# Kernel optimization log

Measured on AMD Instinct MI355X. Metric: run time of the kernel, lower is better.

The kernel has to match this reference:

```python
import jax, jax.numpy as jnp
import numpy as np


def conv2d(x, w, pad=1):
    return jax.lax.conv_general_dilated(
        x, w, (1, 1), [(pad, pad), (pad, pad)],
        dimension_numbers=('NCHW', 'OIHW', 'NCHW'))


def bn(x, g, b, m, v, eps=1e-5):
    inv = g / jnp.sqrt(v + eps)
    return x * inv[None, :, None, None] + (b - m * inv)[None, :, None, None]


def deform_conv(x, wp, bp, wd):
    # v2-style DeformConv2D: internal p_conv -> offsets, bilinear sample, 3x3 conv
    b, c, h, w = x.shape
    ks = 3
    N = ks * ks
    offset = conv2d(x, wp, 1) + bp[None, :, None, None]   # (b, 2N, h, w)
    xp = jnp.pad(x, ((0, 0), (0, 0), (1, 1), (1, 1)))     # zero_padding(1)
    Hp, Wp = h + 2, w + 2
    off = offset.transpose(0, 2, 3, 1)                    # (b, h, w, 2N)
    pn_y, pn_x = jnp.meshgrid(jnp.arange(-1, 2), jnp.arange(-1, 2), indexing='ij')
    # sampling locations p = p_0 + p_n + offset (in padded coords)
    py = jnp.arange(1, h + 1)[None, :, None, None] + pn_y.reshape(-1)[None, None, None, :] + off[..., :N]
    px = jnp.arange(1, w + 1)[None, None, :, None] + pn_x.reshape(-1)[None, None, None, :] + off[..., N:]
    fy = jnp.floor(jax.lax.stop_gradient(py))
    fx = jnp.floor(jax.lax.stop_gradient(px))
    qy0 = jnp.clip(fy, 0, Hp - 1); qy1 = jnp.clip(fy + 1, 0, Hp - 1)
    qx0 = jnp.clip(fx, 0, Wp - 1); qx1 = jnp.clip(fx + 1, 0, Wp - 1)
    py = jnp.clip(py, 0, Hp - 1); px = jnp.clip(px, 0, Wp - 1)
    g_lt = (1 + (qy0 - py)) * (1 + (qx0 - px))
    g_rb = (1 - (qy1 - py)) * (1 - (qx1 - px))
    g_lb = (1 + (qy0 - py)) * (1 - (qx1 - px))
    g_rt = (1 - (qy1 - py)) * (1 + (qx0 - px))
    flat = xp.reshape(b, c, Hp * Wp)

    def gather(qy, qx):
        idx = (qy * Wp + qx).astype(jnp.int32).reshape(b, 1, -1)
        return jnp.take_along_axis(flat, idx, axis=2).reshape(b, c, h, w, N)

    x_off = (g_lt[:, None] * gather(qy0, qx0) + g_rb[:, None] * gather(qy1, qx1)
             + g_lb[:, None] * gather(qy0, qx1) + g_rt[:, None] * gather(qy1, qx0))
    outc = wd.shape[0]
    # equivalent to _reshape_x_offset + Conv2d(kernel=ks, stride=ks)
    return jnp.einsum('bchwn,ocn->bohw', x_off, wd.reshape(outc, c, N))


def setup_inputs() -> dict:
    key = jax.random.key(0)
    ks = jax.random.split(key, 24)
    B, H, W = 256, 28, 28

    def nrm(k, s, sc=1.0):
        return jax.random.normal(k, s, jnp.float32) * sc

    return {
        'x': nrm(ks[0], (B, 3, H, W)),
        'w1': nrm(ks[1], (32, 3, 3, 3), 0.2),
        'g1': jax.random.uniform(ks[2], (32,), jnp.float32) + 0.5,
        'b1': nrm(ks[3], (32,), 0.1),
        'm1': nrm(ks[4], (32,), 0.1),
        'v1': jax.random.uniform(ks[5], (32,), jnp.float32) + 0.5,
        'wp': nrm(ks[6], (18, 32, 3, 3), 0.01),  # p_conv: small offsets
        'bp': nrm(ks[7], (18,), 0.1),
        'w2': nrm(ks[8], (32, 32, 3, 3), 0.1),
        'g2': jax.random.uniform(ks[9], (32,), jnp.float32) + 0.5,
        'b2': nrm(ks[10], (32,), 0.1),
        'm2': nrm(ks[11], (32,), 0.1),
        'v2': jax.random.uniform(ks[12], (32,), jnp.float32) + 0.5,
        'w3': nrm(ks[13], (64, 32, 3, 3), 0.1),
        'g3': jax.random.uniform(ks[14], (64,), jnp.float32) + 0.5,
        'b3': nrm(ks[15], (64,), 0.1),
        'm3': nrm(ks[16], (64,), 0.1),
        'v3': jax.random.uniform(ks[17], (64,), jnp.float32) + 0.5,
        'wc': nrm(ks[18], (10, 64), 0.1),
        'bc': nrm(ks[19], (10,), 0.1),
    }


def reference(x, w1, g1, b1, m1, v1, wp, bp, w2, g2, b2, m2, v2,
              w3, g3, b3, m3, v3, wc, bc):
    h = bn(jax.nn.relu(conv2d(x, w1)), g1, b1, m1, v1)
    h = bn(jax.nn.relu(deform_conv(h, wp, bp, w2)), g2, b2, m2, v2)
    h = bn(jax.nn.relu(conv2d(h, w3)), g3, b3, m3, v3)
    h = h.mean(axis=(2, 3))               # avg_pool2d(28) on 28x28 -> global mean
    logits = h @ wc.T + bc
    return jax.nn.log_softmax(logits, axis=1)
```

## Files before the change

kernel.cpp:

```cpp
#include <hip/hip_runtime.h>
#include <hip/hip_bf16.h>
#include <math.h>

typedef __attribute__((ext_vector_type(8))) short short8;
typedef __attribute__((ext_vector_type(4))) float floatx4;
typedef __attribute__((ext_vector_type(2))) float floatx2;

#define NB 256

#define WPB_OFF 0u
#define W2B_OFF 18432u
#define W3B_OFF 36864u
#define W1B_OFF 73728u
#define C1S_OFF 75776u
#define C2S_OFF 75904u
#define C3S_OFF 76032u

#define L_IMG1 0
#define L_U    50240
#define L_OFFT 100480
#define L_WL   114304
#define L_TOT  152192

static __device__ __forceinline__ unsigned short f2bf(float f) {
    unsigned u = __float_as_uint(f);
    u = (u + 0x7fffu + ((u >> 16) & 1u)) >> 16;
    return (unsigned short)u;
}

static __device__ __forceinline__ unsigned pk2bf(float a, float b) {
    __hip_bfloat162 h = __float22bfloat162_rn(make_float2(a, b));
    unsigned r;
    __builtin_memcpy(&r, &h, 4);
    return r;
}

static __device__ __forceinline__ floatx2 up2(unsigned u) {
    floatx2 r;
    r.x = __uint_as_float(u << 16);
    r.y = __uint_as_float(u & 0xffff0000u);
    return r;
}

__global__ void wcvt(const float* __restrict__ wp, const float* __restrict__ w2,
                     const float* __restrict__ w3, const float* __restrict__ w1,
                     const float* __restrict__ g1, const float* __restrict__ b1,
                     const float* __restrict__ m1, const float* __restrict__ v1,
                     const float* __restrict__ g2, const float* __restrict__ b2,
                     const float* __restrict__ m2, const float* __restrict__ v2,
                     const float* __restrict__ g3, const float* __restrict__ b3,
                     const float* __restrict__ m3, const float* __restrict__ v3,
                     unsigned short* __restrict__ wpb, unsigned short* __restrict__ w2b,
                     unsigned short* __restrict__ w3b, unsigned short* __restrict__ w1b,
                     float* __restrict__ c1s, float* __restrict__ c2s,
                     float* __restrict__ c3s)
{
    int t = blockIdx.x * 256 + threadIdx.x;
    if (t < 9216) {
        int oc = t / 288, k = t % 288;
        int n = k >> 5, ic = k & 31;
        wpb[t] = (oc < 18) ? f2bf(wp[oc * 288 + ic * 9 + n]) : (unsigned short)0;
    } else if (t < 18432) {
        int i = t - 9216;
        int oc = i / 288, k = i % 288;
        int n = k >> 5, ic = k & 31;
        float inv = g2[oc] * rsqrtf(v2[oc] + 1e-5f);
        w2b[i] = f2bf(w2[oc * 288 + ic * 9 + n] * inv);
    } else if (t < 36864) {
        int i = t - 18432;
        int oc = i / 288, k = i % 288;
        int n = k >> 5, ic = k & 31;
        float inv = g3[oc] * rsqrtf(v3[oc] + 1e-5f);
        w3b[i] = f2bf(w3[oc * 288 + ic * 9 + n] * inv);
    } else if (t < 37888) {
        int i = t - 36864;
        int oc = i >> 5, k = i & 31;
        int n = k / 3, ic = k - n * 3;
        float inv = g1[oc] * rsqrtf(v1[oc] + 1e-5f);
        w1b[i] = (k < 27) ? f2bf(w1[oc * 27 + ic * 9 + n] * inv) : (unsigned short)0;
    } else if (t < 37920) {
        int c = t - 37888;
        float inv = g1[c] * rsqrtf(v1[c] + 1e-5f);
        c1s[c] = b1[c] - m1[c] * inv;
    } else if (t < 37952) {
        int c = t - 37920;
        float inv = g2[c] * rsqrtf(v2[c] + 1e-5f);
        c2s[c] = b2[c] - m2[c] * inv;
    } else if (t < 38016) {
        int c = t - 37952;
        float inv = g3[c] * rsqrtf(v3[c] + 1e-5f);
        c3s[c] = b3[c] - m3[c] * inv;
    }
}

__global__ __launch_bounds__(768, 3) void meganet(
    const float* __restrict__ x,
    const unsigned short* __restrict__ wpb, const unsigned short* __restrict__ w2b,
    const unsigned short* __restrict__ w3b, const unsigned short* __restrict__ w1b,
    const float* __restrict__ c1s, const float* __restrict__ c2s,
    const float* __restrict__ c3s, const float* __restrict__ bp,
    const float* __restrict__ wc, const float* __restrict__ bc,
    float* __restrict__ outp)
{
    __shared__ __align__(16) unsigned char ALL[L_TOT];
    int t = threadIdx.x, b = blockIdx.x;
    int w = t >> 6, l = t & 63, col = l & 15, q = l >> 4;

    unsigned char* img1 = ALL + L_IMG1;
    unsigned char* uimg = ALL + L_U;

    {
        const float4* xg = (const float4*)(x + (size_t)b * 2352);
        float4* xl = (float4*)uimg;
        for (int i = t; i < 588; i += 768) xl[i] = xg[i];
    }
    {
        const uint4* s1 = (const uint4*)wpb;
        const uint4* s2 = (const uint4*)w2b;
        for (int i = t; i < 2304; i += 768) {
            int row = i / 36, g = i - row * 36;
            uint4 v = (row < 32) ? s1[row * 36 + g] : s2[(row - 32) * 36 + g];
            *(uint4*)(ALL + L_WL + row * 592 + g * 16) = v;
        }
        if (t < 128) *(uint4*)(ALL + L_OFFT + t * 16) = ((const uint4*)w1b)[t];
    }
    if (t == 700) ((float*)uimg)[2352] = 0.f;
    if (t < 4)  *(uint4*)(img1 + 784 * 64 + t * 16) = make_uint4(0u, 0u, 0u, 0u);
    if (t >= 4 && t < 8) *(uint4*)(uimg + 784 * 64 + (t - 4) * 16) = make_uint4(0u, 0u, 0u, 0u);

    float s0 = c1s[col], s1v = c1s[16 + col];
    float bias0 = bp[col];
    float bias1 = (col < 2) ? bp[16 + col] : 0.f;
    float sh0 = c2s[col], sh1 = c2s[16 + col];

    __syncthreads();

    {
        short8 bf0 = *(const short8*)(ALL + L_OFFT + col * 64 + q * 16);
        short8 bf1 = *(const short8*)(ALL + L_OFFT + (16 + col) * 64 + q * 16);
        const float* xs = (const float*)uimg;
        for (int mt = w; mt < 49; mt += 12) {
            int p = mt * 16 + col;
            int y = p / 28, xx = p % 28;
            unsigned au[4];
#pragma unroll
            for (int jp = 0; jp < 4; jp++) {
                float vv[2];
#pragma unroll
                for (int h = 0; h < 2; h++) {
                    int k = q * 8 + jp * 2 + h;
                    int n = k / 3, ic = k - n * 3;
                    int yy = y + n / 3 - 1, xc = xx + n % 3 - 1;
                    bool ok = (k < 27) && ((unsigned)yy < 28u) && ((unsigned)xc < 28u);
                    int idx = ok ? (ic * 784 + yy * 28 + xc) : 2352;
                    vv[h] = xs[idx];
                }
                au[jp] = pk2bf(vv[0], vv[1]);
            }
            uint4 a4 = make_uint4(au[0], au[1], au[2], au[3]);
            short8 a = *(short8*)&a4;
            floatx4 d0 = {0.f, 0.f, 0.f, 0.f}, d1 = {0.f, 0.f, 0.f, 0.f};
            d0 = __builtin_amdgcn_mfma_f32_16x16x32_bf16(a, bf0, d0, 0, 0, 0);
            d1 = __builtin_amdgcn_mfma_f32_16x16x32_bf16(a, bf1, d1, 0, 0, 0);
#pragma unroll
            for (int r = 0; r < 4; r++) {
                int pout = mt * 16 + q * 4 + r;
                *(unsigned short*)(img1 + pout * 64 + col * 2) = f2bf(fmaxf(d0[r], 0.f) + s0);
                *(unsigned short*)(img1 + pout * 64 + 32 + col * 2) = f2bf(fmaxf(d1[r], 0.f) + s1v);
            }
        }
    }
    __syncthreads();

    {
        const unsigned char* ib = img1;
        float* otw = (float*)(ALL + L_OFFT) + w * 288;

        for (int mt = w; mt < 49; mt += 12) {
            int p = mt * 16 + col;
            int y = p / 28, xx = p % 28;

            floatx4 a0 = {0.f, 0.f, 0.f, 0.f}, a1 = {0.f, 0.f, 0.f, 0.f};
#pragma unroll
            for (int n = 0; n < 9; n++) {
                int yy = y + n / 3 - 1, xc = xx + n % 3 - 1;
                bool ok = ((unsigned)yy < 28u) && ((unsigned)xc < 28u);
                int tp = ok ? (yy * 28 + xc) : 784;
                short8 a  = *(const short8*)(ib + tp * 64 + q * 16);
                short8 p0 = *(const short8*)(ALL + L_WL + col * 592 + n * 64 + q * 16);
                short8 p1 = *(const short8*)(ALL + L_WL + (16 + col) * 592 + n * 64 + q * 16);
                a0 = __builtin_amdgcn_mfma_f32_16x16x32_bf16(a, p0, a0, 0, 0, 0);
                a1 = __builtin_amdgcn_mfma_f32_16x16x32_bf16(a, p1, a1, 0, 0, 0);
            }
#pragma unroll
            for (int r = 0; r < 4; r++)
                otw[(q * 4 + r) * 18 + col] = a0[r] + bias0;
            if (col < 2) {
#pragma unroll
                for (int r = 0; r < 4; r++)
                    otw[(q * 4 + r) * 18 + 16 + col] = a1[r] + bias1;
            }
            __asm__ volatile("s_waitcnt lgkmcnt(0)" ::: "memory");

            floatx4 d0 = {0.f, 0.f, 0.f, 0.f}, d1 = {0.f, 0.f, 0.f, 0.f};
#pragma unroll
            for (int n = 0; n < 9; n++) {
                float offy = otw[col * 18 + n];
                float offx = otw[col * 18 + 9 + n];
                float py = (float)(y + n / 3) + offy;
                float px = (float)(xx + n % 3) + offx;
                float fy = floorf(py), fx = floorf(px);
                float qy0 = fminf(fmaxf(fy, 0.f), 29.f);
                float qy1 = fminf(fmaxf(fy + 1.f, 0.f), 29.f);
                float qx0 = fminf(fmaxf(fx, 0.f), 29.f);
                float qx1 = fminf(fmaxf(fx + 1.f, 0.f), 29.f);
                float pyc = fminf(fmaxf(py, 0.f), 29.f);
                float pxc = fminf(fmaxf(px, 0.f), 29.f);
                float glt = (1.f + (qy0 - pyc)) * (1.f + (qx0 - pxc));
                float grb = (1.f - (qy1 - pyc)) * (1.f - (qx1 - pxc));
                float glb = (1.f + (qy0 - pyc)) * (1.f - (qx1 - pxc));
                float grt = (1.f - (qy1 - pyc)) * (1.f + (qx0 - pxc));
                int iy0 = (int)qy0, iy1 = (int)qy1, ix0 = (int)qx0, ix1 = (int)qx1;
                int ly0 = iy0 - 1, ly1 = iy1 - 1, lx0 = ix0 - 1, lx1 = ix1 - 1;
                bool v00 = ((unsigned)ly0 < 28u) && ((unsigned)lx0 < 28u);
                bool v11 = ((unsigned)ly1 < 28u) && ((unsigned)lx1 < 28u);
                bool v01 = ((unsigned)ly0 < 28u) && ((unsigned)lx1 < 28u);
                bool v10 = ((unsigned)ly1 < 28u) && ((unsigned)lx0 < 28u);
                int p00 = v00 ? (ly0 * 28 + lx0) : 784;
                int p11 = v11 ? (ly1 * 28 + lx1) : 784;
                int p01 = v01 ? (ly0 * 28 + lx1) : 784;
                int p10 = v10 ? (ly1 * 28 + lx0) : 784;
                uint4 u00 = *(const uint4*)(ib + p00 * 64 + q * 16);
                uint4 u11 = *(const uint4*)(ib + p11 * 64 + q * 16);
                uint4 u01 = *(const uint4*)(ib + p01 * 64 + q * 16);
                uint4 u10 = *(const uint4*)(ib + p10 * 64 + q * 16);
                floatx2 f0 = up2(u00.x) * glt + up2(u11.x) * grb + up2(u01.x) * glb + up2(u10.x) * grt;
                floatx2 f1 = up2(u00.y) * glt + up2(u11.y) * grb + up2(u01.y) * glb + up2(u10.y) * grt;
                floatx2 f2 = up2(u00.z) * glt + up2(u11.z) * grb + up2(u01.z) * glb + up2(u10.z) * grt;
                floatx2 f3 = up2(u00.w) * glt + up2(u11.w) * grb + up2(u01.w) * glb + up2(u10.w) * grt;
                uint4 af4 = make_uint4(pk2bf(f0.x, f0.y), pk2bf(f1.x, f1.y),
                                       pk2bf(f2.x, f2.y), pk2bf(f3.x, f3.y));
                short8 af = *(short8*)&af4;
                short8 wb0 = *(const short8*)(ALL + L_WL + (32 + col) * 592 + n * 64 + q * 16);
                short8 wb1 = *(const short8*)(ALL + L_WL + (48 + col) * 592 + n * 64 + q * 16);
                d0 = __builtin_amdgcn_mfma_f32_16x16x32_bf16(af, wb0, d0, 0, 0, 0);
                d1 = __builtin_amdgcn_mfma_f32_16x16x32_bf16(af, wb1, d1, 0, 0, 0);
            }
#pragma unroll
            for (int r = 0; r < 4; r++) {
                int pout = mt * 16 + q * 4 + r;
                *(unsigned short*)(uimg + pout * 64 + col * 2) = f2bf(fmaxf(d0[r], 0.f) + sh0);
                *(unsigned short*)(uimg + pout * 64 + 32 + col * 2) = f2bf(fmaxf(d1[r], 0.f) + sh1);
            }
        }
    }
    __syncthreads();

    {
        const uint4* src = (const uint4*)w3b;
        for (int i = t; i < 2304; i += 768) {
            int row = i / 36, g = i - row * 36;
            *(uint4*)(ALL + L_WL + row * 592 + g * 16) = src[row * 36 + g];
        }
    }
    __syncthreads();

    {
        float* part = (float*)(ALL + L_OFFT);
        int ocp = w & 1;
        const unsigned char* ib = uimg;
        float psA = 0.f, psB = 0.f;
        for (int mt = (w >> 1); mt < 49; mt += 6) {
            int p = mt * 16 + col;
            int y = p / 28, xx = p % 28;
            floatx4 cA = {0.f, 0.f, 0.f, 0.f}, cB = {0.f, 0.f, 0.f, 0.f};
#pragma unroll
            for (int n = 0; n < 9; n++) {
                int yy = y + n / 3 - 1, xc = xx + n % 3 - 1;
                bool ok = ((unsigned)yy < 28u) && ((unsigned)xc < 28u);
                int tp = ok ? (yy * 28 + xc) : 784;
                short8 a  = *(const short8*)(ib + tp * 64 + q * 16);
                short8 wA = *(const short8*)(ALL + L_WL + (ocp * 32 + col) * 592 + n * 64 + q * 16);
                short8 wB = *(const short8*)(ALL + L_WL + (ocp * 32 + 16 + col) * 592 + n * 64 + q * 16);
                cA = __builtin_amdgcn_mfma_f32_16x16x32_bf16(a, wA, cA, 0, 0, 0);
                cB = __builtin_amdgcn_mfma_f32_16x16x32_bf16(a, wB, cB, 0, 0, 0);
            }
            psA += fmaxf(cA[0], 0.f) + fmaxf(cA[1], 0.f) + fmaxf(cA[2], 0.f) + fmaxf(cA[3], 0.f);
            psB += fmaxf(cB[0], 0.f) + fmaxf(cB[1], 0.f) + fmaxf(cB[2], 0.f) + fmaxf(cB[3], 0.f);
        }
        psA += __shfl_xor(psA, 16, 64); psA += __shfl_xor(psA, 32, 64);
        psB += __shfl_xor(psB, 16, 64); psB += __shfl_xor(psB, 32, 64);
        if (l < 16) { part[w * 32 + l] = psA; part[w * 32 + 16 + l] = psB; }
    }
    __syncthreads();

    if (t < 64) {
        const float* part = (const float*)(ALL + L_OFFT);
        int hi = t >> 5, c = t & 31;
        float s = 0.f;
#pragma unroll
        for (int j = 0; j < 6; j++) s += part[(2 * j + hi) * 32 + c];
        float feat = s * (1.f / 784.f) + c3s[t];
        float lg[10];
        float mx = -1e30f;
#pragma unroll
        for (int j = 0; j < 10; j++) {
            float v = feat * wc[j * 64 + t];
            v += __shfl_xor(v, 1, 64);  v += __shfl_xor(v, 2, 64);
            v += __shfl_xor(v, 4, 64);  v += __shfl_xor(v, 8, 64);
            v += __shfl_xor(v, 16, 64); v += __shfl_xor(v, 32, 64);
            lg[j] = v + bc[j];
            mx = fmaxf(mx, lg[j]);
        }
        float se = 0.f;
#pragma unroll
        for (int j = 0; j < 10; j++) se += expf(lg[j] - mx);
        float lse = logf(se);
#pragma unroll
        for (int j = 0; j < 10; j++)
            if (t == j) outp[(size_t)b * 10 + j] = lg[j] - mx - lse;
    }
}

extern "C" void kernel_launch(void* const* d_in, const int* in_sizes, int n_in,
                              void* d_out, int out_size, void* d_ws, size_t ws_size,
                              hipStream_t stream)
{
    (void)in_sizes; (void)n_in; (void)out_size; (void)ws_size;
    const float* x  = (const float*)d_in[0];
    const float* w1 = (const float*)d_in[1];
    const float* g1 = (const float*)d_in[2];
    const float* b1 = (const float*)d_in[3];
    const float* m1 = (const float*)d_in[4];
    const float* v1 = (const float*)d_in[5];
    const float* wp = (const float*)d_in[6];
    const float* bp = (const float*)d_in[7];
    const float* w2 = (const float*)d_in[8];
    const float* g2 = (const float*)d_in[9];
    const float* b2 = (const float*)d_in[10];
    const float* m2 = (const float*)d_in[11];
    const float* v2 = (const float*)d_in[12];
    const float* w3 = (const float*)d_in[13];
    const float* g3 = (const float*)d_in[14];
    const float* b3 = (const float*)d_in[15];
    const float* m3 = (const float*)d_in[16];
    const float* v3 = (const float*)d_in[17];
    const float* wc = (const float*)d_in[18];
    const float* bc = (const float*)d_in[19];
    float* outp = (float*)d_out;

    unsigned char* ws = (unsigned char*)d_ws;
    unsigned short* wpb = (unsigned short*)(ws + WPB_OFF);
    unsigned short* w2b = (unsigned short*)(ws + W2B_OFF);
    unsigned short* w3b = (unsigned short*)(ws + W3B_OFF);
    unsigned short* w1b = (unsigned short*)(ws + W1B_OFF);
    float* c1s = (float*)(ws + C1S_OFF);
    float* c2s = (float*)(ws + C2S_OFF);
    float* c3s = (float*)(ws + C3S_OFF);

    wcvt<<<149, 256, 0, stream>>>(wp, w2, w3, w1, g1, b1, m1, v1,
                                  g2, b2, m2, v2, g3, b3, m3, v3,
                                  wpb, w2b, w3b, w1b, c1s, c2s, c3s);
    meganet<<<NB, 768, 0, stream>>>(x, wpb, w2b, w3b, w1b, c1s, c2s, c3s,
                                    bp, wc, bc, outp);
}
```

Measured before the change: 138.5 us.

## Deduplicate bilinear coordinate math across quad lanes via LDS records

```diff
diff --git a/kernel.cpp b/kernel.cpp
--- a/kernel.cpp
+++ b/kernel.cpp
@@ -19,8 +19,8 @@
 #define L_IMG1 0
 #define L_U    50240
 #define L_OFFT 100480
-#define L_WL   114304
-#define L_TOT  152192
+#define L_WL   125056
+#define L_TOT  162944
 
 static __device__ __forceinline__ unsigned short f2bf(float f) {
     unsigned u = __float_as_uint(f);
@@ -39,6 +39,22 @@
     floatx2 r;
     r.x = __uint_as_float(u << 16);
     r.y = __uint_as_float(u & 0xffff0000u);
+    return r;
+}
+
+static __device__ __forceinline__ unsigned pkh(float a, float b) {
+    _Float16 ha = (_Float16)a, hb = (_Float16)b;
+    unsigned short ua, ub;
+    __builtin_memcpy(&ua, &ha, 2);
+    __builtin_memcpy(&ub, &hb, 2);
+    return (unsigned)ua | ((unsigned)ub << 16);
+}
+static __device__ __forceinline__ floatx2 uph(unsigned u) {
+    unsigned short lo = (unsigned short)(u & 0xffffu), hi = (unsigned short)(u >> 16);
+    _Float16 hl, hh;
+    __builtin_memcpy(&hl, &lo, 2);
+    __builtin_memcpy(&hh, &hi, 2);
+    floatx2 r; r.x = (float)hl; r.y = (float)hh;
     return r;
 }
 
@@ -174,7 +190,9 @@
 
     {
         const unsigned char* ib = img1;
-        float* otw = (float*)(ALL + L_OFFT) + w * 288;
+        unsigned char* wsc = ALL + L_OFFT + w * 2048;
+        float* otw = (float*)wsc;
+        unsigned char* gscr = wsc + 1152;
 
         for (int mt = w; mt < 49; mt += 12) {
             int p = mt * 16 + col;
@@ -204,47 +222,66 @@
 
             floatx4 d0 = {0.f, 0.f, 0.f, 0.f}, d1 = {0.f, 0.f, 0.f, 0.f};
 #pragma unroll
-            for (int n = 0; n < 9; n++) {
-                float offy = otw[col * 18 + n];
-                float offx = otw[col * 18 + 9 + n];
-                float py = (float)(y + n / 3) + offy;
-                float px = (float)(xx + n % 3) + offx;
-                float fy = floorf(py), fx = floorf(px);
-                float qy0 = fminf(fmaxf(fy, 0.f), 29.f);
-                float qy1 = fminf(fmaxf(fy + 1.f, 0.f), 29.f);
-                float qx0 = fminf(fmaxf(fx, 0.f), 29.f);
-                float qx1 = fminf(fmaxf(fx + 1.f, 0.f), 29.f);
-                float pyc = fminf(fmaxf(py, 0.f), 29.f);
-                float pxc = fminf(fmaxf(px, 0.f), 29.f);
-                float glt = (1.f + (qy0 - pyc)) * (1.f + (qx0 - pxc));
-                float grb = (1.f - (qy1 - pyc)) * (1.f - (qx1 - pxc));
-                float glb = (1.f + (qy0 - pyc)) * (1.f - (qx1 - pxc));
-                float grt = (1.f - (qy1 - pyc)) * (1.f + (qx0 - pxc));
-                int iy0 = (int)qy0, iy1 = (int)qy1, ix0 = (int)qx0, ix1 = (int)qx1;
-                int ly0 = iy0 - 1, ly1 = iy1 - 1, lx0 = ix0 - 1, lx1 = ix1 - 1;
-                bool v00 = ((unsigned)ly0 < 28u) && ((unsigned)lx0 < 28u);
-                bool v11 = ((unsigned)ly1 < 28u) && ((unsigned)lx1 < 28u);
-                bool v01 = ((unsigned)ly0 < 28u) && ((unsigned)lx1 < 28u);
-                bool v10 = ((unsigned)ly1 < 28u) && ((unsigned)lx0 < 28u);
-                int p00 = v00 ? (ly0 * 28 + lx0) : 784;
-                int p11 = v11 ? (ly1 * 28 + lx1) : 784;
-                int p01 = v01 ? (ly0 * 28 + lx1) : 784;
-                int p10 = v10 ? (ly1 * 28 + lx0) : 784;
-                uint4 u00 = *(const uint4*)(ib + p00 * 64 + q * 16);
-                uint4 u11 = *(const uint4*)(ib + p11 * 64 + q * 16);
-                uint4 u01 = *(const uint4*)(ib + p01 * 64 + q * 16);
-                uint4 u10 = *(const uint4*)(ib + p10 * 64 + q * 16);
-                floatx2 f0 = up2(u00.x) * glt + up2(u11.x) * grb + up2(u01.x) * glb + up2(u10.x) * grt;
-                floatx2 f1 = up2(u00.y) * glt + up2(u11.y) * grb + up2(u01.y) * glb + up2(u10.y) * grt;
-                floatx2 f2 = up2(u00.z) * glt + up2(u11.z) * grb + up2(u01.z) * glb + up2(u10.z) * grt;
-                floatx2 f3 = up2(u00.w) * glt + up2(u11.w) * grb + up2(u01.w) * glb + up2(u10.w) * grt;
-                uint4 af4 = make_uint4(pk2bf(f0.x, f0.y), pk2bf(f1.x, f1.y),
-                                       pk2bf(f2.x, f2.y), pk2bf(f3.x, f3.y));
-                short8 af = *(short8*)&af4;
-                short8 wb0 = *(const short8*)(ALL + L_WL + (32 + col) * 592 + n * 64 + q * 16);
-                short8 wb1 = *(const short8*)(ALL + L_WL + (48 + col) * 592 + n * 64 + q * 16);
-                d0 = __builtin_amdgcn_mfma_f32_16x16x32_bf16(af, wb0, d0, 0, 0, 0);
-                d1 = __builtin_amdgcn_mfma_f32_16x16x32_bf16(af, wb1, d1, 0, 0, 0);
+            for (int tg = 0; tg < 3; tg++) {
+                if (l < 48) {
+                    int px = l & 15, n = tg * 3 + (l >> 4);
+                    int pg = mt * 16 + px;
+                    int yg = pg / 28, xg = pg % 28;
+                    float offy = otw[px * 18 + n];
+                    float offx = otw[px * 18 + 9 + n];
+                    float py = (float)(yg + n / 3) + offy;
+                    float pxf = (float)(xg + n % 3) + offx;
+                    float fy = floorf(py), fx = floorf(pxf);
+                    float qy0 = fminf(fmaxf(fy, 0.f), 29.f);
+                    float qy1 = fminf(fmaxf(fy + 1.f, 0.f), 29.f);
+                    float qx0 = fminf(fmaxf(fx, 0.f), 29.f);
+                    float qx1 = fminf(fmaxf(fx + 1.f, 0.f), 29.f);
+                    float pyc = fminf(fmaxf(py, 0.f), 29.f);
+                    float pxc = fminf(fmaxf(pxf, 0.f), 29.f);
+                    float glt = (1.f + (qy0 - pyc)) * (1.f + (qx0 - pxc));
+                    float grb = (1.f - (qy1 - pyc)) * (1.f - (qx1 - pxc));
+                    float glb = (1.f + (qy0 - pyc)) * (1.f - (qx1 - pxc));
+                    float grt = (1.f - (qy1 - pyc)) * (1.f + (qx0 - pxc));
+                    int iy0 = (int)qy0, iy1 = (int)qy1, ix0 = (int)qx0, ix1 = (int)qx1;
+                    int ly0 = iy0 - 1, ly1 = iy1 - 1, lx0 = ix0 - 1, lx1 = ix1 - 1;
+                    bool v00 = ((unsigned)ly0 < 28u) && ((unsigned)lx0 < 28u);
+                    bool v11 = ((unsigned)ly1 < 28u) && ((unsigned)lx1 < 28u);
+                    bool v01 = ((unsigned)ly0 < 28u) && ((unsigned)lx1 < 28u);
+                    bool v10 = ((unsigned)ly1 < 28u) && ((unsigned)lx0 < 28u);
+                    unsigned p00 = v00 ? (unsigned)(ly0 * 28 + lx0) : 784u;
+                    unsigned p11 = v11 ? (unsigned)(ly1 * 28 + lx1) : 784u;
+                    unsigned p01 = v01 ? (unsigned)(ly0 * 28 + lx1) : 784u;
+                    unsigned p10 = v10 ? (unsigned)(ly1 * 28 + lx0) : 784u;
+                    uint4 rec = make_uint4(pkh(glt, grb), pkh(glb, grt),
+                                           p00 | (p11 << 16), p01 | (p10 << 16));
+                    *(uint4*)(gscr + l * 16) = rec;
+                }
+                __asm__ volatile("s_waitcnt lgkmcnt(0)" ::: "memory");
+
+#pragma unroll
+                for (int k3 = 0; k3 < 3; k3++) {
+                    int n = tg * 3 + k3;
+                    uint4 rec = *(const uint4*)(gscr + (k3 * 16 + col) * 16);
+                    floatx2 gA = uph(rec.x), gB = uph(rec.y);
+                    float glt = gA.x, grb = gA.y, glb = gB.x, grt = gB.y;
+                    int p00 = (int)(rec.z & 0xffffu), p11 = (int)(rec.z >> 16);
+                    int p01 = (int)(rec.w & 0xffffu), p10 = (int)(rec.w >> 16);
+                    uint4 u00 = *(const uint4*)(ib + p00 * 64 + q * 16);
+                    uint4 u11 = *(const uint4*)(ib + p11 * 64 + q * 16);
+                    uint4 u01 = *(const uint4*)(ib + p01 * 64 + q * 16);
+                    uint4 u10 = *(const uint4*)(ib + p10 * 64 + q * 16);
+                    floatx2 f0 = up2(u00.x) * glt + up2(u11.x) * grb + up2(u01.x) * glb + up2(u10.x) * grt;
+                    floatx2 f1 = up2(u00.y) * glt + up2(u11.y) * grb + up2(u01.y) * glb + up2(u10.y) * grt;
+                    floatx2 f2 = up2(u00.z) * glt + up2(u11.z) * grb + up2(u01.z) * glb + up2(u10.z) * grt;
+                    floatx2 f3 = up2(u00.w) * glt + up2(u11.w) * grb + up2(u01.w) * glb + up2(u10.w) * grt;
+                    uint4 af4 = make_uint4(pk2bf(f0.x, f0.y), pk2bf(f1.x, f1.y),
+                                           pk2bf(f2.x, f2.y), pk2bf(f3.x, f3.y));
+                    short8 af = *(short8*)&af4;
+                    short8 wb0 = *(const short8*)(ALL + L_WL + (32 + col) * 592 + n * 64 + q * 16);
+                    short8 wb1 = *(const short8*)(ALL + L_WL + (48 + col) * 592 + n * 64 + q * 16);
+                    d0 = __builtin_amdgcn_mfma_f32_16x16x32_bf16(af, wb0, d0, 0, 0, 0);
+                    d1 = __builtin_amdgcn_mfma_f32_16x16x32_bf16(af, wb1, d1, 0, 0, 0);
+                }
             }
 #pragma unroll
             for (int r = 0; r < 4; r++) {
```

New measurement: 134.2 us. -3.1%, faster.
